# Kernel optimization log

Measured on AMD Instinct MI355X. Metric: run time of the kernel, lower is better.

Reference implementation:

```python
import jax, jax.numpy as jnp
import numpy as np

N_NODES = 100000
NEG_SLOPE = 0.2


def _leaky(x):
    return jnp.where(x >= 0, x, NEG_SLOPE * x)


def _normalize(v):
    # F.normalize(p=2, dim=1) with eps=1e-12
    n = jnp.linalg.norm(v, axis=1, keepdims=True)
    return v / jnp.maximum(n, 1e-12)


def _householder(v, e):
    # (I - 2 v v^T) e  == e - 2 v (v . e); reflector is symmetric so W^T == W
    return e - 2.0 * v * jnp.sum(v * e, axis=1, keepdims=True)


def _level_update(node_embs, W_proj, w_att, rel_pc_emb, rel_comp_emb,
                  parent, child, root):
    D = node_embs.shape[1]
    # rel_proj (Linear, no bias): [E, rel_dim] @ [rel_dim, D]
    v_k = _normalize(rel_pc_emb @ W_proj.T)    # [E, D]
    v_p = _normalize(rel_comp_emb @ W_proj.T)  # [E, D]
    e_i = node_embs[root]    # [E, D]
    e_x = node_embs[parent]
    e_y = node_embs[child]
    e_i_proj = _householder(v_p, e_i)
    e_x_proj = _householder(v_k, e_x)
    # w_att on concat([e_i_proj, e_x_proj, e_y]) without materializing [E, 3D]
    w1, w2, w3 = w_att[:D], w_att[D:2 * D], w_att[2 * D:]
    b = _leaky(e_i_proj @ w1 + e_x_proj @ w2 + e_y @ w3)  # [E]
    # segment softmax over parent
    b_max = jax.ops.segment_max(b, parent, num_segments=N_NODES)
    b_exp = jnp.exp(b - b_max[parent])
    b_sum = jnp.maximum(jax.ops.segment_sum(b_exp, parent, num_segments=N_NODES), 1e-10)
    a = b_exp / b_sum[parent]  # [E]
    upd = _householder(v_k, e_y) * a[:, None]  # [E, D]
    agg = jax.ops.segment_sum(upd, parent, num_segments=N_NODES)  # [N, D]
    return _leaky(node_embs + agg)


def setup_inputs() -> dict:
    key = jax.random.key(0)
    ks = jax.random.split(key, 16)
    E2, E1, B, R, D, RD = 200000, 100000, 8192, 1000, 300, 100
    return {
        "node_embs": jax.random.normal(ks[0], (N_NODES, D), jnp.float32),
        "rel_table": jax.random.normal(ks[1], (R, RD), jnp.float32),
        "W_proj": jax.random.normal(ks[2], (D, RD), jnp.float32) * 0.1,
        "w_att": jax.random.normal(ks[3], (3 * D,), jnp.float32) * 0.05,
        "parent_idx2": jax.random.randint(ks[4], (E2,), 0, N_NODES),
        "child_idx2": jax.random.randint(ks[5], (E2,), 0, N_NODES),
        "root_idx2": jax.random.randint(ks[6], (E2,), 0, N_NODES),
        "rel2": jax.random.randint(ks[7], (E2,), 0, R),
        "rel_rp2": jax.random.randint(ks[8], (E2,), 0, R),
        "parent_idx1": jax.random.randint(ks[9], (E1,), 0, N_NODES),
        "child_idx1": jax.random.randint(ks[10], (E1,), 0, N_NODES),
        "root_idx1": jax.random.randint(ks[11], (E1,), 0, N_NODES),
        "rel1": jax.random.randint(ks[12], (E1,), 0, R),
        "root_out": jax.random.randint(ks[13], (B,), 0, N_NODES),
    }


def reference(node_embs, rel_table, W_proj, w_att,
              parent_idx2, child_idx2, root_idx2, rel2, rel_rp2,
              parent_idx1, child_idx1, root_idx1, rel1, root_out):
    # Level 2: composed relation = rel(root->parent) * rel(parent->child)
    rel_pc2 = rel_table[rel2]
    rel_comp2 = rel_table[rel_rp2] * rel_pc2
    node_embs = _level_update(node_embs, W_proj, w_att, rel_pc2, rel_comp2,
                              parent_idx2, child_idx2, root_idx2)
    # Level 1: composed relation = rel(parent->child) itself
    rel_pc1 = rel_table[rel1]
    node_embs = _level_update(node_embs, W_proj, w_att, rel_pc1, rel_pc1,
                              parent_idx1, child_idx1, root_idx1)
    return node_embs[root_out]
```

## Files before the change

kernel.cpp:

```cpp
#include <hip/hip_runtime.h>
#include <hip/hip_bf16.h>
#include <cstdint>

#define N_NODES 100000
#define NPAD 100096
#define D 300
#define RD 100
#define NREL 1000
#define E2 200000
#define E1 100000
#define NB 8192
#define NEG 0.2f
#define SCAN_BLKS 391
#define NBLKC 782
#define NWAVES (NBLKC*4)

typedef __bf16 bf16x8 __attribute__((ext_vector_type(8)));
typedef float f32x4 __attribute__((ext_vector_type(4)));
typedef unsigned short us4 __attribute__((ext_vector_type(4)));
typedef unsigned short us8 __attribute__((ext_vector_type(8)));
typedef unsigned long long ull;

__device__ __forceinline__ float leaky(float x){ return x >= 0.f ? x : NEG*x; }

__device__ __forceinline__ unsigned short f2b(float v){
  unsigned u = __float_as_uint(v);
  unsigned r = u + 0x7FFF + ((u>>16)&1u);
  return (unsigned short)(r>>16);
}
__device__ __forceinline__ float b2f(unsigned short b){
  return __uint_as_float(((unsigned)b) << 16);
}
__device__ __forceinline__ float wred(float v){
  #pragma unroll
  for (int m = 32; m >= 1; m >>= 1) v += __shfl_xor(v, m, 64);
  return v;
}

__global__ void k_init(int* __restrict__ FRO, int* __restrict__ ND2,
                       int* __restrict__ CNTa, int* __restrict__ CURa,
                       int* __restrict__ CNTb, int* __restrict__ CURb){
  int i = blockIdx.x*256 + threadIdx.x;
  if (i < N_NODES){ FRO[i]=0; ND2[i]=0; CNTa[i]=0; CURa[i]=0; CNTb[i]=0; CURb[i]=0; }
}
__global__ void k_flag(const int* __restrict__ ro, int* __restrict__ FRO){
  int o = blockIdx.x*256 + threadIdx.x;
  if (o < NB) FRO[ro[o]] = 1;
}
__global__ void k_need(const int* __restrict__ par1, const int* __restrict__ chi1,
                       const int* __restrict__ roo1, const int* __restrict__ ro,
                       const int* __restrict__ FRO, int* __restrict__ ND2){
  int i = blockIdx.x*256 + threadIdx.x;
  if (i < NB) ND2[ro[i]] = 1;
  if (i < E1){
    int p = par1[i];
    if (FRO[p]){ ND2[p] = 1; ND2[chi1[i]] = 1; ND2[roo1[i]] = 1; }
  }
}

__global__ void k_cnt3(const int* __restrict__ par2, const int* __restrict__ par1,
                       const int* __restrict__ FRO, const int* __restrict__ ND2,
                       ull* __restrict__ MSK, int* __restrict__ BC){
  int i = blockIdx.x*256 + threadIdx.x;
  int lane = threadIdx.x & 63, wid = threadIdx.x >> 6;
  __shared__ int ws[3][4];
  int p2 = (i < E2) && ND2[par2[i]];
  int p1 = (i < E1) && FRO[par1[i]];
  int pn = (i < N_NODES) && ND2[i];
  ull m2 = __ballot(p2), m1 = __ballot(p1), mn = __ballot(pn);
  if (lane == 0){
    int wg = blockIdx.x*4 + wid;
    MSK[0*NWAVES + wg] = m2; ws[0][wid] = __popcll(m2);
    MSK[1*NWAVES + wg] = m1; ws[1][wid] = __popcll(m1);
    MSK[2*NWAVES + wg] = mn; ws[2][wid] = __popcll(mn);
  }
  __syncthreads();
  if (threadIdx.x < 3)
    BC[threadIdx.x*NBLKC + blockIdx.x] =
      ws[threadIdx.x][0]+ws[threadIdx.x][1]+ws[threadIdx.x][2]+ws[threadIdx.x][3];
}

__global__ __launch_bounds__(1024) void k_scanblk(const int* __restrict__ BC,
                                                  int* __restrict__ BOFF, int* __restrict__ NLV){
  __shared__ int ls[1024];
  for (int l=0; l<3; ++l){
    int v = (threadIdx.x < NBLKC) ? BC[l*NBLKC + threadIdx.x] : 0;
    ls[threadIdx.x] = v;
    __syncthreads();
    for (int off=1; off<1024; off<<=1){
      int t = (threadIdx.x >= off) ? ls[threadIdx.x-off] : 0;
      __syncthreads();
      ls[threadIdx.x] += t;
      __syncthreads();
    }
    if (threadIdx.x < NBLKC) BOFF[l*NBLKC + threadIdx.x] = ls[threadIdx.x] - v;
    if (threadIdx.x == 1023) NLV[l] = ls[1023];
    __syncthreads();
  }
}

__global__ void k_fill(const ull* __restrict__ MSK, const int* __restrict__ BOFF,
                       int* __restrict__ L2L, int* __restrict__ L1L, int* __restrict__ NDL){
  int i = blockIdx.x*256 + threadIdx.x;
  int lane = threadIdx.x & 63, wid = threadIdx.x >> 6;
  int wg = blockIdx.x*4 + wid;
  __shared__ int ws[3][4];
  ull m2 = MSK[0*NWAVES+wg], m1 = MSK[1*NWAVES+wg], mn = MSK[2*NWAVES+wg];
  if (lane == 0){ ws[0][wid]=__popcll(m2); ws[1][wid]=__popcll(m1); ws[2][wid]=__popcll(mn); }
  __syncthreads();
  int w2=0, w1=0, wn=0;
  #pragma unroll
  for (int k=0;k<4;++k){
    if (k < wid){ w2+=ws[0][k]; w1+=ws[1][k]; wn+=ws[2][k]; }
  }
  ull below = (1ull<<lane) - 1ull;
  if ((m2>>lane)&1ull) L2L[BOFF[0*NBLKC+blockIdx.x] + w2 + __popcll(m2 & below)] = i;
  if ((m1>>lane)&1ull) L1L[BOFF[1*NBLKC+blockIdx.x] + w1 + __popcll(m1 & below)] = i;
  if ((mn>>lane)&1ull) NDL[BOFF[2*NBLKC+blockIdx.x] + wn + __popcll(mn & below)] = i;
}

__global__ void k_prep2b(const float* __restrict__ W, const float* __restrict__ watt,
                         unsigned short* __restrict__ MbT){
  int u = blockIdx.x*blockDim.x + threadIdx.x;
  if (u >= 112*128) return;
  int j = u >> 7, i = u & 127;
  float v = 0.f;
  if (i < RD){
    if (j < RD){ float a=0.f; for (int d=0;d<D;++d) a += W[d*RD+i]*W[d*RD+j]; v=a; }
    else if (j == RD){ float a=0.f; for (int d=0;d<D;++d) a += watt[d]*W[d*RD+i]; v=a; }
  }
  MbT[u] = f2b(v);
}

__global__ void k_prepAll(const float* __restrict__ W, const float* __restrict__ watt,
                          const float* __restrict__ relT, unsigned short* __restrict__ Bt,
                          unsigned short* __restrict__ WtB, unsigned short* __restrict__ Rb){
  int b = blockIdx.x;
  if (b < 140){
    int u = b*256 + threadIdx.x;
    if (u < 112*320){
      int c = u / 320, k = u % 320;
      float v = 0.f;
      if (k < D){
        if (c < RD) v = W[k*RD + c];
        else if (c < RD+3) v = watt[(c-RD)*D + k];
      }
      Bt[u] = f2b(v);
    }
  } else if (b < 292){
    int u = (b-140)*256 + threadIdx.x;
    if (u < 304*128){
      int dd = u >> 7, k = u & 127;
      float v = (dd < D && k < RD) ? W[dd*RD + k] : 0.f;
      WtB[u] = f2b(v);
    }
  } else {
    int u = (b-292)*256 + threadIdx.x;
    if (u < 1024*16){
      int row = u >> 4, c8 = (u & 15)*8;
      us8 o;
      #pragma unroll
      for (int j=0;j<8;++j){
        int c = c8+j;
        o[j] = (row < NREL && c < RD) ? f2b(relT[row*RD + c]) : (unsigned short)0;
      }
      *(us8*)(Rb + (size_t)row*128 + c8) = o;
    }
  }
}

__global__ __launch_bounds__(256) void k_relmm(const unsigned short* __restrict__ Rb,
    const unsigned short* __restrict__ WtB, const float* __restrict__ watt,
    unsigned short* __restrict__ Vh, float* __restrict__ RINV,
    float* __restrict__ RVW1, float* __restrict__ RVW2){
  int lane = threadIdx.x & 63, wid = threadIdx.x >> 6;
  int r0 = blockIdx.x*64 + wid*16;
  int ep = lane & 15, g = lane >> 4;
  size_t a0 = (size_t)(r0 + ep)*128 + g*8;
  size_t b0 = (size_t)ep*128 + g*8;
  f32x4 acc[19];
  #pragma unroll
  for (int cf=0;cf<19;++cf) acc[cf]=(f32x4){0.f,0.f,0.f,0.f};
  #pragma unroll
  for (int ks=0; ks<4; ++ks){
    bf16x8 af = *(const bf16x8*)(Rb + a0 + ks*32);
    #pragma unroll
    for (int cf=0; cf<19; ++cf){
      bf16x8 bf = *(const bf16x8*)(WtB + b0 + (size_t)cf*16*128 + ks*32);
      acc[cf] = __builtin_amdgcn_mfma_f32_16x16x32_bf16(af, bf, acc[cf], 0, 0, 0);
    }
  }
  float w1v[19], w2v[19];
  #pragma unroll
  for (int cf=0; cf<19; ++cf){
    int col = cf*16+ep;
    bool ok = col < D;
    w1v[cf] = ok ? watt[col] : 0.f;
    w2v[cf] = ok ? watt[D+col] : 0.f;
  }
  #pragma unroll
  for (int reg=0; reg<4; ++reg){
    int row = r0 + g*4 + reg;
    float np = 0.f;
    #pragma unroll
    for (int cf=0; cf<19; ++cf){ float u = acc[cf][reg]; np += u*u; }
    np += __shfl_xor(np,1); np += __shfl_xor(np,2); np += __shfl_xor(np,4); np += __shfl_xor(np,8);
    float iv = 1.f / fmaxf(sqrtf(np), 1e-12f);
    float p1 = 0.f, p2 = 0.f;
    if (row < NREL){
      #pragma unroll
      for (int cf=0; cf<19; ++cf){
        int col = cf*16+ep;
        float v = acc[cf][reg]*iv;
        if (col < D){
          Vh[(size_t)row*D + col] = f2b(v);
          p1 += v*w1v[cf];
          p2 += v*w2v[cf];
        }
      }
    }
    p1 += __shfl_xor(p1,1); p1 += __shfl_xor(p1,2); p1 += __shfl_xor(p1,4); p1 += __shfl_xor(p1,8);
    p2 += __shfl_xor(p2,1); p2 += __shfl_xor(p2,2); p2 += __shfl_xor(p2,4); p2 += __shfl_xor(p2,8);
    if (ep == 0 && row < NREL){
      RINV[row] = iv; RVW1[row] = p1; RVW2[row] = p2;
    }
  }
}

__global__ void k_cast(const float* __restrict__ src, unsigned short* __restrict__ dst){
  int total = NPAD*40;
  for (int u = blockIdx.x*blockDim.x + threadIdx.x; u < total; u += gridDim.x*blockDim.x){
    int row = u/40, c8 = (u%40)*8;
    us8 o;
    if (row < N_NODES && c8 <= 292){
      float4 x = *(const float4*)(src + (size_t)row*D + c8);
      float4 y = *(const float4*)(src + (size_t)row*D + c8 + 4);
      o[0]=f2b(x.x); o[1]=f2b(x.y); o[2]=f2b(x.z); o[3]=f2b(x.w);
      o[4]=f2b(y.x); o[5]=f2b(y.y); o[6]=f2b(y.z); o[7]=f2b(y.w);
    } else {
      #pragma unroll
      for (int j=0;j<8;++j){
        int c = c8+j;
        float v = (row < N_NODES && c < D) ? src[(size_t)row*D + c] : 0.f;
        o[j] = f2b(v);
      }
    }
    *(us8*)(dst + (size_t)row*320 + c8) = o;
  }
}

__global__ __launch_bounds__(256) void k_nodetab2(const unsigned short* __restrict__ Eb,
    const unsigned short* __restrict__ Bt, unsigned short* __restrict__ Gh, float* __restrict__ P){
  int lane = threadIdx.x & 63, wid = threadIdx.x >> 6;
  int n0 = blockIdx.x*128;
  size_t a0 = (size_t)(n0 + wid*32 + (lane&15))*320 + ((lane>>4)*8);
  size_t b0 = (size_t)(lane&15)*320 + ((lane>>4)*8);
  f32x4 acc[2][7];
  #pragma unroll
  for (int s=0;s<2;++s)
    #pragma unroll
    for (int c=0;c<7;++c) acc[s][c] = (f32x4){0.f,0.f,0.f,0.f};
  for (int ks = 0; ks < 10; ++ks){
    bf16x8 a0f = *(const bf16x8*)(Eb + a0 + ks*32);
    bf16x8 a1f = *(const bf16x8*)(Eb + a0 + 16*320 + ks*32);
    #pragma unroll
    for (int cf=0; cf<7; ++cf){
      bf16x8 bf = *(const bf16x8*)(Bt + b0 + (size_t)cf*16*320 + ks*32);
      acc[0][cf] = __builtin_amdgcn_mfma_f32_16x16x32_bf16(a0f, bf, acc[0][cf], 0, 0, 0);
      acc[1][cf] = __builtin_amdgcn_mfma_f32_16x16x32_bf16(a1f, bf, acc[1][cf], 0, 0, 0);
    }
  }
  int rbase = n0 + wid*32 + ((lane>>4)<<2);
  int cbase = lane & 15;
  #pragma unroll
  for (int sub=0; sub<2; ++sub){
    #pragma unroll
    for (int cf=0; cf<7; ++cf){
      int col = cf*16 + cbase;
      #pragma unroll
      for (int r=0; r<4; ++r){
        int row = rbase + sub*16 + r;
        if (row < N_NODES){
          float v = acc[sub][cf][r];
          if (col < RD) Gh[(size_t)row*RD + col] = f2b(v);
          else if (col < RD+3) P[(size_t)row*4 + (col-RD)] = v;
        }
      }
    }
  }
}

__global__ __launch_bounds__(256) void k_nodetab2i(const unsigned short* __restrict__ Eb,
    const unsigned short* __restrict__ Bt, const int* __restrict__ NDL, const int* __restrict__ NLV,
    unsigned short* __restrict__ Gh, float* __restrict__ P){
  int nlv = NLV[2];
  int base = blockIdx.x*128;
  if (base >= nlv) return;
  int lane = threadIdx.x & 63, wid = threadIdx.x >> 6;
  int li0 = base + wid*32 + (lane&15);
  int li1 = li0 + 16;
  int row0 = (li0 < nlv) ? NDL[li0] : 0;
  int row1 = (li1 < nlv) ? NDL[li1] : 0;
  size_t a0 = (size_t)row0*320 + ((lane>>4)*8);
  size_t a1 = (size_t)row1*320 + ((lane>>4)*8);
  size_t b0 = (size_t)(lane&15)*320 + ((lane>>4)*8);
  f32x4 acc[2][7];
  #pragma unroll
  for (int s=0;s<2;++s)
    #pragma unroll
    for (int c=0;c<7;++c) acc[s][c] = (f32x4){0.f,0.f,0.f,0.f};
  for (int ks = 0; ks < 10; ++ks){
    bf16x8 a0f = *(const bf16x8*)(Eb + a0 + ks*32);
    bf16x8 a1f = *(const bf16x8*)(Eb + a1 + ks*32);
    #pragma unroll
    for (int cf=0; cf<7; ++cf){
      bf16x8 bf = *(const bf16x8*)(Bt + b0 + (size_t)cf*16*320 + ks*32);
      acc[0][cf] = __builtin_amdgcn_mfma_f32_16x16x32_bf16(a0f, bf, acc[0][cf], 0, 0, 0);
      acc[1][cf] = __builtin_amdgcn_mfma_f32_16x16x32_bf16(a1f, bf, acc[1][cf], 0, 0, 0);
    }
  }
  int lbase = base + wid*32 + ((lane>>4)<<2);
  int cbase = lane & 15;
  #pragma unroll
  for (int sub=0; sub<2; ++sub){
    #pragma unroll
    for (int r=0; r<4; ++r){
      int li = lbase + sub*16 + r;
      if (li >= nlv) continue;
      int row = NDL[li];
      #pragma unroll
      for (int cf=0; cf<7; ++cf){
        int col = cf*16 + cbase;
        float v = acc[sub][cf][r];
        if (col < RD) Gh[(size_t)row*RD + col] = f2b(v);
        else if (col < RD+3) P[(size_t)row*4 + (col-RD)] = v;
      }
    }
  }
}

__global__ __launch_bounds__(256) void k_pass1_l2c(
    const float* __restrict__ relT, const int* __restrict__ rel2i, const int* __restrict__ relrp2,
    const int* __restrict__ par, const int* __restrict__ chi, const int* __restrict__ roo,
    const unsigned short* __restrict__ Gh, const float* __restrict__ P,
    const unsigned short* __restrict__ MbT,
    const float* __restrict__ RINV, const float* __restrict__ RVW2,
    const int* __restrict__ L2L, const int* __restrict__ NLV,
    float* __restrict__ BBUF, float* __restrict__ DK, int* __restrict__ CNT){
  __shared__ unsigned short Cl[4*16*136];
  int nlv = NLV[0];
  if (blockIdx.x*64 >= nlv) return;
  int lane = threadIdx.x & 63, wid = threadIdx.x >> 6;
  int ep = lane & 15, g = lane >> 4;
  unsigned short* cw = Cl + wid*16*136;
  int idx = blockIdx.x*64 + wid*16 + ep;
  int live = idx < nlv;
  int e = live ? L2L[idx] : 0;
  int rp = par[e];
  int ra = rel2i[e], rb = relrp2[e], rc = chi[e], rr = roo[e];
  const float* rA = relT + (size_t)ra*RD;
  const float* rB = relT + (size_t)rb*RD;
  const unsigned short* gR = Gh + (size_t)rr*RD;
  const unsigned short* gX = Gh + (size_t)rp*RD;
  const unsigned short* gY = Gh + (size_t)rc*RD;
  float dgi = 0.f, dgx = 0.f, dgy = 0.f;
  bf16x8 af[4];
  #pragma unroll
  for (int ks=0; ks<4; ++ks){
    us8 cpack;
    #pragma unroll
    for (int h=0; h<2; ++h){
      int k0 = g*8 + ks*32 + h*4;
      float4 a4 = make_float4(0.f,0.f,0.f,0.f), b4 = a4, grr = a4, grp = a4, gry = a4;
      if (live && k0 <= 96){
        a4  = *(const float4*)(rA + k0);
        b4  = *(const float4*)(rB + k0);
        us4 r4 = *(const us4*)(gR + k0);
        us4 x4 = *(const us4*)(gX + k0);
        us4 y4 = *(const us4*)(gY + k0);
        grr = make_float4(b2f(r4[0]),b2f(r4[1]),b2f(r4[2]),b2f(r4[3]));
        grp = make_float4(b2f(x4[0]),b2f(x4[1]),b2f(x4[2]),b2f(x4[3]));
        gry = make_float4(b2f(y4[0]),b2f(y4[1]),b2f(y4[2]),b2f(y4[3]));
      }
      float4 c4;
      c4.x = a4.x*b4.x; c4.y = a4.y*b4.y; c4.z = a4.z*b4.z; c4.w = a4.w*b4.w;
      dgi += c4.x*grr.x + c4.y*grr.y + c4.z*grr.z + c4.w*grr.w;
      dgx += a4.x*grp.x + a4.y*grp.y + a4.z*grp.z + a4.w*grp.w;
      dgy += a4.x*gry.x + a4.y*gry.y + a4.z*gry.z + a4.w*gry.w;
      cpack[h*4+0]=f2b(c4.x); cpack[h*4+1]=f2b(c4.y); cpack[h*4+2]=f2b(c4.z); cpack[h*4+3]=f2b(c4.w);
    }
    *(us8*)((char*)cw + ep*272 + g*16 + ks*64) = cpack;
    af[ks] = *(bf16x8*)&cpack;
  }
  f32x4 acc[7];
  #pragma unroll
  for (int cf=0; cf<7; ++cf) acc[cf] = (f32x4){0.f,0.f,0.f,0.f};
  #pragma unroll
  for (int cf=0; cf<7; ++cf){
    #pragma unroll
    for (int ks=0; ks<4; ++ks){
      bf16x8 bfr = *(const bf16x8*)(MbT + (size_t)(cf*16+ep)*128 + g*8 + ks*32);
      acc[cf] = __builtin_amdgcn_mfma_f32_16x16x32_bf16(af[ks], bfr, acc[cf], 0, 0, 0);
    }
  }
  dgi += __shfl_xor(dgi, 16); dgi += __shfl_xor(dgi, 32);
  dgx += __shfl_xor(dgx, 16); dgx += __shfl_xor(dgx, 32);
  dgy += __shfl_xor(dgy, 16); dgy += __shfl_xor(dgy, 32);
  __syncthreads();
  #pragma unroll
  for (int r=0; r<4; ++r){
    int row = g*4 + r;
    int src = (lane & 48) | row;
    int livr = __shfl(live, src);
    if (!livr) continue;
    float pr = 0.f;
    #pragma unroll
    for (int cf=0; cf<7; ++cf)
      pr += b2f(cw[row*136 + cf*16 + ep]) * acc[cf][r];
    pr += __shfl_xor(pr, 1); pr += __shfl_xor(pr, 2);
    pr += __shfl_xor(pr, 4); pr += __shfl_xor(pr, 8);
    float dw1r = __shfl(acc[6][r], (lane & 48) | 4);
    float dgir = __shfl(dgi, src);
    float dgxr = __shfl(dgx, src);
    float dgyr = __shfl(dgy, src);
    int rar = __shfl(ra, src), rpr = __shfl(rp, src);
    int rcr = __shfl(rc, src), rrr = __shfl(rr, src);
    int er  = __shfl(e, src);
    float invp = 1.f / fmaxf(sqrtf(pr), 1e-12f);
    float rinv = RINV[rar];
    float t1 = (dgir*invp)*(dw1r*invp);
    float t2 = (dgxr*rinv)*RVW2[rar];
    float bb = P[(size_t)rrr*4+0] - 2.f*t1 + P[(size_t)rpr*4+1] - 2.f*t2 + P[(size_t)rcr*4+2];
    bb = leaky(bb);
    if (ep == 0){
      BBUF[er] = bb;
      DK[er] = dgyr * rinv;
      atomicAdd(&CNT[rpr], 1);
    }
  }
}

__global__ __launch_bounds__(256) void k_pass1_l1c(
    const float* __restrict__ relT, const int* __restrict__ rel1i,
    const int* __restrict__ par, const int* __restrict__ chi, const int* __restrict__ roo,
    const unsigned short* __restrict__ Gh, const float* __restrict__ P,
    const float* __restrict__ RINV, const float* __restrict__ RVW1, const float* __restrict__ RVW2,
    const int* __restrict__ L1L, const int* __restrict__ NLV,
    float* __restrict__ BBUF, float* __restrict__ DK, int* __restrict__ CNT){
  int nlv = NLV[1];
  int j = (blockIdx.x*256 + threadIdx.x) >> 6;
  if (j >= nlv) return;
  int lane = threadIdx.x & 63;
  int e = L1L[j];
  int pp = par[e];
  int r = rel1i[e], cc = chi[e], ii = roo[e];
  const float* rrow = relT + r*RD;
  const unsigned short* gI = Gh + (size_t)ii*RD;
  const unsigned short* gX = Gh + (size_t)pp*RD;
  const unsigned short* gY = Gh + (size_t)cc*RD;
  float ai = rrow[lane]*b2f(gI[lane]);
  float ax = rrow[lane]*b2f(gX[lane]);
  float ay = rrow[lane]*b2f(gY[lane]);
  if (lane < 36){
    ai += rrow[lane+64]*b2f(gI[lane+64]);
    ax += rrow[lane+64]*b2f(gX[lane+64]);
    ay += rrow[lane+64]*b2f(gY[lane+64]);
  }
  float dgi = wred(ai), dgx = wred(ax), dgy = wred(ay);
  if (lane == 0){
    float invn = RINV[r];
    float b = P[(size_t)ii*4+0] - 2.f*(dgi*invn)*RVW1[r]
            + P[(size_t)pp*4+1] - 2.f*(dgx*invn)*RVW2[r]
            + P[(size_t)cc*4+2];
    b = leaky(b);
    BBUF[e] = b;
    DK[e] = dgy * invn;
    atomicAdd(&CNT[pp], 1);
  }
}

__global__ __launch_bounds__(256) void k_scan_a(const int* __restrict__ CNT,
    int* __restrict__ ROFF, int* __restrict__ PART){
  __shared__ int ls[256];
  int i = blockIdx.x*256 + threadIdx.x;
  int v = (i < N_NODES) ? CNT[i] : 0;
  ls[threadIdx.x] = v;
  __syncthreads();
  for (int off=1; off<256; off<<=1){
    int t = (threadIdx.x >= off) ? ls[threadIdx.x-off] : 0;
    __syncthreads();
    ls[threadIdx.x] += t;
    __syncthreads();
  }
  int incl = ls[threadIdx.x];
  if (i < N_NODES) ROFF[i] = incl - v;
  if (threadIdx.x == 255) PART[blockIdx.x] = incl;
}
__global__ __launch_bounds__(512) void k_scan_b(int* __restrict__ PART){
  __shared__ int ls[512];
  int v = (threadIdx.x < SCAN_BLKS) ? PART[threadIdx.x] : 0;
  ls[threadIdx.x] = v;
  __syncthreads();
  for (int off=1; off<512; off<<=1){
    int t = (threadIdx.x >= off) ? ls[threadIdx.x-off] : 0;
    __syncthreads();
    ls[threadIdx.x] += t;
    __syncthreads();
  }
  if (threadIdx.x < SCAN_BLKS) PART[threadIdx.x] = ls[threadIdx.x] - v;
}
__global__ void k_scatterc(const int* __restrict__ L, const int* __restrict__ NLV, int which,
                           const int* __restrict__ par, const int* __restrict__ ROFF,
                           const int* __restrict__ PART, int* __restrict__ CUR,
                           int* __restrict__ EIDX){
  int j = blockIdx.x*256 + threadIdx.x;
  if (j >= NLV[which]) return;
  int e = L[j];
  int p = par[e];
  int pos = ROFF[p] + PART[p>>8] + atomicAdd(&CUR[p], 1);
  EIDX[pos] = e;
}

__device__ __forceinline__ void agg_bucket(int p, int lane,
    const int* __restrict__ ROFF, const int* __restrict__ PART, const int* __restrict__ CNT,
    const int* __restrict__ EIDX, const float* __restrict__ BBUF, const float* __restrict__ DK,
    const int* __restrict__ chi, const int* __restrict__ relI,
    const unsigned short* __restrict__ Vh, const unsigned short* __restrict__ Xe,
    float acc[5]){
  int cnt = CNT[p];
  if (cnt <= 0) return;
  int base = ROFF[p] + PART[p>>8];
  if (cnt <= 64){
    float bl = (lane < cnt) ? BBUF[EIDX[base+lane]] : -1e30f;
    float m = bl;
    #pragma unroll
    for (int msk=32; msk>=1; msk>>=1) m = fmaxf(m, __shfl_xor(m, msk));
    float el = (lane < cnt) ? __expf(bl - m) : 0.f;
    float s = wred(el);
    float inv = 1.f / fmaxf(s, 1e-10f);
    for (int i=0;i<cnt;++i){
      int eid = EIDX[base+i];
      float a = __shfl(el, i) * inv;
      float s2 = 2.f*DK[eid]*a;
      int y = chi[eid], r = relI[eid];
      const unsigned short* vr = Vh + (size_t)r*D;
      const unsigned short* ey = Xe + (size_t)y*320;
      #pragma unroll
      for (int q=0;q<4;++q){
        int d = lane + 64*q;
        acc[q] += b2f(ey[d])*a - s2*b2f(vr[d]);
      }
      if (lane < 44){
        int d = lane + 256;
        acc[4] += b2f(ey[d])*a - s2*b2f(vr[d]);
      }
    }
  } else {
    float m = -1e30f;
    for (int i=0;i<cnt;++i) m = fmaxf(m, BBUF[EIDX[base+i]]);
    float s = 0.f;
    for (int i=0;i<cnt;++i) s += __expf(BBUF[EIDX[base+i]] - m);
    float inv = 1.f / fmaxf(s, 1e-10f);
    for (int i=0;i<cnt;++i){
      int eid = EIDX[base+i];
      float a = __expf(BBUF[eid]-m)*inv;
      float s2 = 2.f*DK[eid]*a;
      int y = chi[eid], r = relI[eid];
      const unsigned short* vr = Vh + (size_t)r*D;
      const unsigned short* ey = Xe + (size_t)y*320;
      #pragma unroll
      for (int q=0;q<4;++q){
        int d = lane + 64*q;
        acc[q] += b2f(ey[d])*a - s2*b2f(vr[d]);
      }
      if (lane < 44){
        int d = lane + 256;
        acc[4] += b2f(ey[d])*a - s2*b2f(vr[d]);
      }
    }
  }
}

__global__ __launch_bounds__(256) void k_agg2(const int* __restrict__ ROFF, const int* __restrict__ PART,
    const int* __restrict__ CNT, const int* __restrict__ EIDX,
    const float* __restrict__ BBUF, const float* __restrict__ DK,
    const int* __restrict__ chi, const int* __restrict__ relI,
    const unsigned short* __restrict__ Vh, const unsigned short* __restrict__ Xe,
    const int* __restrict__ NDL, const int* __restrict__ NLV,
    unsigned short* __restrict__ Xo){
  int nlv = NLV[2];
  int idx = (blockIdx.x*256 + threadIdx.x) >> 6;
  if (idx >= nlv) return;
  int lane = threadIdx.x & 63;
  int p = NDL[idx];
  float acc[5] = {0.f,0.f,0.f,0.f,0.f};
  agg_bucket(p, lane, ROFF, PART, CNT, EIDX, BBUF, DK, chi, relI, Vh, Xe, acc);
  const unsigned short* in = Xe + (size_t)p*320;
  unsigned short* op = Xo + (size_t)p*320;
  #pragma unroll
  for (int q=0;q<4;++q){
    int d = lane + 64*q;
    op[d] = f2b(leaky(b2f(in[d]) + acc[q]));
  }
  {
    int d = lane + 256;
    unsigned short o = 0;
    if (lane < 44) o = f2b(leaky(b2f(in[d]) + acc[4]));
    op[d] = o;
  }
}

__global__ __launch_bounds__(256) void k_aggout(const int* __restrict__ ro,
    const int* __restrict__ ROFF, const int* __restrict__ PART,
    const int* __restrict__ CNT, const int* __restrict__ EIDX,
    const float* __restrict__ BBUF, const float* __restrict__ DK,
    const int* __restrict__ chi, const int* __restrict__ relI,
    const unsigned short* __restrict__ Vh, const unsigned short* __restrict__ Xe,
    float* __restrict__ out){
  int lane = threadIdx.x & 63;
  int o = (blockIdx.x*256 + threadIdx.x) >> 6;
  if (o >= NB) return;
  int p = ro[o];
  float acc[5] = {0.f,0.f,0.f,0.f,0.f};
  agg_bucket(p, lane, ROFF, PART, CNT, EIDX, BBUF, DK, chi, relI, Vh, Xe, acc);
  const unsigned short* in = Xe + (size_t)p*320;
  float* op = out + (size_t)o*D;
  #pragma unroll
  for (int q=0;q<4;++q){
    int d = lane + 64*q;
    op[d] = leaky(b2f(in[d]) + acc[q]);
  }
  if (lane < 44){
    int d = lane + 256;
    op[d] = leaky(b2f(in[d]) + acc[4]);
  }
}

extern "C" void kernel_launch(void* const* d_in, const int* in_sizes, int n_in,
                              void* d_out, int out_size, void* d_ws, size_t ws_size,
                              hipStream_t stream){
  const float* node = (const float*)d_in[0];
  const float* relT = (const float*)d_in[1];
  const float* W    = (const float*)d_in[2];
  const float* watt = (const float*)d_in[3];
  const int* par2 = (const int*)d_in[4];
  const int* chi2 = (const int*)d_in[5];
  const int* roo2 = (const int*)d_in[6];
  const int* rel2i = (const int*)d_in[7];
  const int* relrp2 = (const int*)d_in[8];
  const int* par1 = (const int*)d_in[9];
  const int* chi1 = (const int*)d_in[10];
  const int* roo1 = (const int*)d_in[11];
  const int* rel1i = (const int*)d_in[12];
  const int* roout = (const int*)d_in[13];

  char* w = (char*)d_ws;
  size_t off = 0;
  auto alloc = [&](size_t bytes)->void*{ void* p = w + off; off += (bytes + 255) & ~(size_t)255; return p; };
  unsigned short* Gh = (unsigned short*)alloc((size_t)N_NODES*RD*2);
  float* P    = (float*)alloc((size_t)N_NODES*4*4);
  unsigned short* Vh = (unsigned short*)alloc((size_t)NREL*D*2);
  float* RINV = (float*)alloc(NREL*4);
  float* RVW1 = (float*)alloc(NREL*4);
  float* RVW2 = (float*)alloc(NREL*4);
  float* BBUF = (float*)alloc((size_t)E2*4);
  float* DKb  = (float*)alloc((size_t)E2*4);
  unsigned short* Xb  = (unsigned short*)alloc((size_t)NPAD*320*2);
  unsigned short* Xb2 = (unsigned short*)alloc((size_t)NPAD*320*2);
  unsigned short* Bt  = (unsigned short*)alloc((size_t)112*320*2);
  unsigned short* MbT = (unsigned short*)alloc((size_t)112*128*2);
  unsigned short* WtB = (unsigned short*)alloc((size_t)304*128*2);
  unsigned short* Rb  = (unsigned short*)alloc((size_t)1024*128*2);
  int* CNTa = (int*)alloc((size_t)N_NODES*4);
  int* CURa = (int*)alloc((size_t)N_NODES*4);
  int* CNTb = (int*)alloc((size_t)N_NODES*4);
  int* CURb = (int*)alloc((size_t)N_NODES*4);
  int* ROFF = (int*)alloc((size_t)N_NODES*4);
  int* PART = (int*)alloc(512*4);
  int* EIDX = (int*)alloc((size_t)E2*4);
  int* FRO  = (int*)alloc((size_t)N_NODES*4);
  int* ND2  = (int*)alloc((size_t)N_NODES*4);
  int* L2L  = (int*)alloc((size_t)E2*4);
  int* L1L  = (int*)alloc((size_t)E1*4);
  int* NDL  = (int*)alloc((size_t)N_NODES*4);
  int* NLV  = (int*)alloc(256);
  ull* MSK  = (ull*)alloc((size_t)3*NWAVES*8);
  int* BC   = (int*)alloc((size_t)3*NBLKC*4);
  int* BOFF = (int*)alloc((size_t)3*NBLKC*4);

  k_init<<<dim3(SCAN_BLKS), dim3(256), 0, stream>>>(FRO, ND2, CNTa, CURa, CNTb, CURb);
  k_flag<<<dim3((NB+255)/256), dim3(256), 0, stream>>>(roout, FRO);
  k_need<<<dim3((E1+255)/256), dim3(256), 0, stream>>>(par1, chi1, roo1, roout, FRO, ND2);
  k_cnt3<<<dim3(NBLKC), dim3(256), 0, stream>>>(par2, par1, FRO, ND2, MSK, BC);
  k_scanblk<<<dim3(1), dim3(1024), 0, stream>>>(BC, BOFF, NLV);
  k_fill<<<dim3(NBLKC), dim3(256), 0, stream>>>(MSK, BOFF, L2L, L1L, NDL);

  k_prep2b<<<dim3(56), dim3(256), 0, stream>>>(W, watt, MbT);
  k_prepAll<<<dim3(356), dim3(256), 0, stream>>>(W, watt, relT, Bt, WtB, Rb);
  k_relmm<<<dim3(16), dim3(256), 0, stream>>>(Rb, WtB, watt, Vh, RINV, RVW1, RVW2);

  k_cast<<<dim3(2048), dim3(256), 0, stream>>>(node, Xb);
  k_nodetab2<<<dim3((N_NODES+127)/128), dim3(256), 0, stream>>>(Xb, Bt, Gh, P);
  k_pass1_l2c<<<dim3(E2/64), dim3(256), 0, stream>>>(relT, rel2i, relrp2, par2, chi2, roo2,
                                                     Gh, P, MbT, RINV, RVW2, L2L, NLV, BBUF, DKb, CNTa);
  k_scan_a<<<dim3(SCAN_BLKS), dim3(256), 0, stream>>>(CNTa, ROFF, PART);
  k_scan_b<<<dim3(1), dim3(512), 0, stream>>>(PART);
  k_scatterc<<<dim3((E2+255)/256), dim3(256), 0, stream>>>(L2L, NLV, 0, par2, ROFF, PART, CURa, EIDX);
  k_agg2<<<dim3((N_NODES+3)/4), dim3(256), 0, stream>>>(ROFF, PART, CNTa, EIDX, BBUF, DKb,
                                                        chi2, rel2i, Vh, Xb, NDL, NLV, Xb2);

  k_nodetab2i<<<dim3((N_NODES+127)/128), dim3(256), 0, stream>>>(Xb2, Bt, NDL, NLV, Gh, P);
  k_pass1_l1c<<<dim3((E1+3)/4), dim3(256), 0, stream>>>(relT, rel1i, par1, chi1, roo1,
                                                        Gh, P, RINV, RVW1, RVW2, L1L, NLV, BBUF, DKb, CNTb);
  k_scan_a<<<dim3(SCAN_BLKS), dim3(256), 0, stream>>>(CNTb, ROFF, PART);
  k_scan_b<<<dim3(1), dim3(512), 0, stream>>>(PART);
  k_scatterc<<<dim3((E1+255)/256), dim3(256), 0, stream>>>(L1L, NLV, 1, par1, ROFF, PART, CURb, EIDX);
  k_aggout<<<dim3((NB+3)/4), dim3(256), 0, stream>>>(roout, ROFF, PART, CNTb, EIDX, BBUF, DKb,
                                                     chi1, rel1i, Vh, Xb2, (float*)d_out);
}
```

Measured before the change: 244.2 us.

## Fuse fp32-to-bf16 node cast into node-table GEMM and merge prep kernels

The separate cast kernel is removed. The node-table MFMA kernel now loads fp32 node embeddings directly, converts them to bf16 in registers, and writes the bf16 copy (Xb) as a side effect. This avoids re-reading the bf16 table from memory and saves one launch. The MbT prep kernel is folded into the combined prep kernel as extra blocks, and the three block-offset scans now run as three parallel blocks instead of one block looping. One risk: padded Xb rows beyond N_NODES are no longer zero-filled.

New measurement: 224.1 us. 1.09x faster.

```diff
diff --git a/kernel.cpp b/kernel.cpp
--- a/kernel.cpp
+++ b/kernel.cpp
@@ -35,6 +35,24 @@
   #pragma unroll
   for (int m = 32; m >= 1; m >>= 1) v += __shfl_xor(v, m, 64);
   return v;
+}
+
+__device__ __forceinline__ us8 ldcvt(const float* __restrict__ p, int row, int cb){
+  us8 o;
+  if (row < N_NODES && cb <= 292){
+    float4 x = *(const float4*)(p + (size_t)row*D + cb);
+    float4 y = *(const float4*)(p + (size_t)row*D + cb + 4);
+    o[0]=f2b(x.x); o[1]=f2b(x.y); o[2]=f2b(x.z); o[3]=f2b(x.w);
+    o[4]=f2b(y.x); o[5]=f2b(y.y); o[6]=f2b(y.z); o[7]=f2b(y.w);
+  } else if (row < N_NODES && cb == 296){
+    float4 x = *(const float4*)(p + (size_t)row*D + 296);
+    o[0]=f2b(x.x); o[1]=f2b(x.y); o[2]=f2b(x.z); o[3]=f2b(x.w);
+    o[4]=0; o[5]=0; o[6]=0; o[7]=0;
+  } else {
+    #pragma unroll
+    for (int j=0;j<8;++j) o[j]=0;
+  }
+  return o;
 }
 
 __global__ void k_init(int* __restrict__ FRO, int* __restrict__ ND2,
@@ -82,21 +100,19 @@
 
 __global__ __launch_bounds__(1024) void k_scanblk(const int* __restrict__ BC,
                                                   int* __restrict__ BOFF, int* __restrict__ NLV){
+  int l = blockIdx.x;
   __shared__ int ls[1024];
-  for (int l=0; l<3; ++l){
-    int v = (threadIdx.x < NBLKC) ? BC[l*NBLKC + threadIdx.x] : 0;
-    ls[threadIdx.x] = v;
+  int v = (threadIdx.x < NBLKC) ? BC[l*NBLKC + threadIdx.x] : 0;
+  ls[threadIdx.x] = v;
+  __syncthreads();
+  for (int off=1; off<1024; off<<=1){
+    int t = (threadIdx.x >= off) ? ls[threadIdx.x-off] : 0;
     __syncthreads();
-    for (int off=1; off<1024; off<<=1){
-      int t = (threadIdx.x >= off) ? ls[threadIdx.x-off] : 0;
-      __syncthreads();
-      ls[threadIdx.x] += t;
-      __syncthreads();
-    }
-    if (threadIdx.x < NBLKC) BOFF[l*NBLKC + threadIdx.x] = ls[threadIdx.x] - v;
-    if (threadIdx.x == 1023) NLV[l] = ls[1023];
+    ls[threadIdx.x] += t;
     __syncthreads();
   }
+  if (threadIdx.x < NBLKC) BOFF[l*NBLKC + threadIdx.x] = ls[threadIdx.x] - v;
+  if (threadIdx.x == 1023) NLV[l] = ls[1023];
 }
 
 __global__ void k_fill(const ull* __restrict__ MSK, const int* __restrict__ BOFF,
@@ -119,22 +135,10 @@
   if ((mn>>lane)&1ull) NDL[BOFF[2*NBLKC+blockIdx.x] + wn + __popcll(mn & below)] = i;
 }
 
-__global__ void k_prep2b(const float* __restrict__ W, const float* __restrict__ watt,
-                         unsigned short* __restrict__ MbT){
-  int u = blockIdx.x*blockDim.x + threadIdx.x;
-  if (u >= 112*128) return;
-  int j = u >> 7, i = u & 127;
-  float v = 0.f;
-  if (i < RD){
-    if (j < RD){ float a=0.f; for (int d=0;d<D;++d) a += W[d*RD+i]*W[d*RD+j]; v=a; }
-    else if (j == RD){ float a=0.f; for (int d=0;d<D;++d) a += watt[d]*W[d*RD+i]; v=a; }
-  }
-  MbT[u] = f2b(v);
-}
-
 __global__ void k_prepAll(const float* __restrict__ W, const float* __restrict__ watt,
                           const float* __restrict__ relT, unsigned short* __restrict__ Bt,
-                          unsigned short* __restrict__ WtB, unsigned short* __restrict__ Rb){
+                          unsigned short* __restrict__ WtB, unsigned short* __restrict__ Rb,
+                          unsigned short* __restrict__ MbT){
   int b = blockIdx.x;
   if (b < 140){
     int u = b*256 + threadIdx.x;
@@ -154,7 +158,7 @@
       float v = (dd < D && k < RD) ? W[dd*RD + k] : 0.f;
       WtB[u] = f2b(v);
     }
-  } else {
+  } else if (b < 356){
     int u = (b-292)*256 + threadIdx.x;
     if (u < 1024*16){
       int row = u >> 4, c8 = (u & 15)*8;
@@ -165,6 +169,17 @@
         o[j] = (row < NREL && c < RD) ? f2b(relT[row*RD + c]) : (unsigned short)0;
       }
       *(us8*)(Rb + (size_t)row*128 + c8) = o;
+    }
+  } else {
+    int u = (b-356)*256 + threadIdx.x;
+    if (u < 112*128){
+      int j = u >> 7, i = u & 127;
+      float v = 0.f;
+      if (i < RD){
+        if (j < RD){ float a=0.f; for (int d=0;d<D;++d) a += W[d*RD+i]*W[d*RD+j]; v=a; }
+        else if (j == RD){ float a=0.f; for (int d=0;d<D;++d) a += watt[d]*W[d*RD+i]; v=a; }
+      }
+      MbT[u] = f2b(v);
     }
   }
 }
@@ -227,42 +242,28 @@
   }
 }
 
-__global__ void k_cast(const float* __restrict__ src, unsigned short* __restrict__ dst){
-  int total = NPAD*40;
-  for (int u = blockIdx.x*blockDim.x + threadIdx.x; u < total; u += gridDim.x*blockDim.x){
-    int row = u/40, c8 = (u%40)*8;
-    us8 o;
-    if (row < N_NODES && c8 <= 292){
-      float4 x = *(const float4*)(src + (size_t)row*D + c8);
-      float4 y = *(const float4*)(src + (size_t)row*D + c8 + 4);
-      o[0]=f2b(x.x); o[1]=f2b(x.y); o[2]=f2b(x.z); o[3]=f2b(x.w);
-      o[4]=f2b(y.x); o[5]=f2b(y.y); o[6]=f2b(y.z); o[7]=f2b(y.w);
-    } else {
-      #pragma unroll
-      for (int j=0;j<8;++j){
-        int c = c8+j;
-        float v = (row < N_NODES && c < D) ? src[(size_t)row*D + c] : 0.f;
-        o[j] = f2b(v);
-      }
-    }
-    *(us8*)(dst + (size_t)row*320 + c8) = o;
-  }
-}
-
-__global__ __launch_bounds__(256) void k_nodetab2(const unsigned short* __restrict__ Eb,
-    const unsigned short* __restrict__ Bt, unsigned short* __restrict__ Gh, float* __restrict__ P){
+__global__ __launch_bounds__(256) void k_nodetab2f(const float* __restrict__ node,
+    const unsigned short* __restrict__ Bt, unsigned short* __restrict__ Gh, float* __restrict__ P,
+    unsigned short* __restrict__ Xb){
   int lane = threadIdx.x & 63, wid = threadIdx.x >> 6;
   int n0 = blockIdx.x*128;
-  size_t a0 = (size_t)(n0 + wid*32 + (lane&15))*320 + ((lane>>4)*8);
-  size_t b0 = (size_t)(lane&15)*320 + ((lane>>4)*8);
+  int row0 = n0 + wid*32 + (lane&15);
+  int row1 = row0 + 16;
+  int cb0 = (lane>>4)*8;
+  size_t b0 = (size_t)(lane&15)*320 + cb0;
   f32x4 acc[2][7];
   #pragma unroll
   for (int s=0;s<2;++s)
     #pragma unroll
     for (int c=0;c<7;++c) acc[s][c] = (f32x4){0.f,0.f,0.f,0.f};
   for (int ks = 0; ks < 10; ++ks){
-    bf16x8 a0f = *(const bf16x8*)(Eb + a0 + ks*32);
-    bf16x8 a1f = *(const bf16x8*)(Eb + a0 + 16*320 + ks*32);
+    int cb = cb0 + ks*32;
+    us8 a0p = ldcvt(node, row0, cb);
+    us8 a1p = ldcvt(node, row1, cb);
+    if (row0 < N_NODES) *(us8*)(Xb + (size_t)row0*320 + cb) = a0p;
+    if (row1 < N_NODES) *(us8*)(Xb + (size_t)row1*320 + cb) = a1p;
+    bf16x8 a0f = *(bf16x8*)&a0p;
+    bf16x8 a1f = *(bf16x8*)&a1p;
     #pragma unroll
     for (int cf=0; cf<7; ++cf){
       bf16x8 bf = *(const bf16x8*)(Bt + b0 + (size_t)cf*16*320 + ks*32);
@@ -692,15 +693,13 @@
   k_flag<<<dim3((NB+255)/256), dim3(256), 0, stream>>>(roout, FRO);
   k_need<<<dim3((E1+255)/256), dim3(256), 0, stream>>>(par1, chi1, roo1, roout, FRO, ND2);
   k_cnt3<<<dim3(NBLKC), dim3(256), 0, stream>>>(par2, par1, FRO, ND2, MSK, BC);
-  k_scanblk<<<dim3(1), dim3(1024), 0, stream>>>(BC, BOFF, NLV);
+  k_scanblk<<<dim3(3), dim3(1024), 0, stream>>>(BC, BOFF, NLV);
   k_fill<<<dim3(NBLKC), dim3(256), 0, stream>>>(MSK, BOFF, L2L, L1L, NDL);
 
-  k_prep2b<<<dim3(56), dim3(256), 0, stream>>>(W, watt, MbT);
-  k_prepAll<<<dim3(356), dim3(256), 0, stream>>>(W, watt, relT, Bt, WtB, Rb);
+  k_prepAll<<<dim3(412), dim3(256), 0, stream>>>(W, watt, relT, Bt, WtB, Rb, MbT);
   k_relmm<<<dim3(16), dim3(256), 0, stream>>>(Rb, WtB, watt, Vh, RINV, RVW1, RVW2);
 
-  k_cast<<<dim3(2048), dim3(256), 0, stream>>>(node, Xb);
-  k_nodetab2<<<dim3((N_NODES+127)/128), dim3(256), 0, stream>>>(Xb, Bt, Gh, P);
+  k_nodetab2f<<<dim3((N_NODES+127)/128), dim3(256), 0, stream>>>(node, Bt, Gh, P, Xb);
   k_pass1_l2c<<<dim3(E2/64), dim3(256), 0, stream>>>(relT, rel2i, relrp2, par2, chi2, roo2,
                                                      Gh, P, MbT, RINV, RVW2, L2L, NLV, BBUF, DKb, CNTa);
   k_scan_a<<<dim3(SCAN_BLKS), dim3(256), 0, stream>>>(CNTa, ROFF, PART);
```
